# Kernel tuning notes

Measured on AMD Instinct MI355X. Metric: run time of the kernel, lower is better.

## Reference

```python
import jax, jax.numpy as jnp
import numpy as np

N_EMBD = 1024
HEAD_SIZE = 64
BLOCK = 4096
B = 4

def setup_inputs() -> dict:
    key = jax.random.key(0)
    k1, k2, k3, k4, k5, k6 = jax.random.split(key, 6)
    x = jax.random.normal(k1, (B, BLOCK, N_EMBD), dtype=jnp.float32)
    freqs_cos = jax.random.uniform(k2, (BLOCK, HEAD_SIZE // 2), dtype=jnp.float32)
    freqs_sin = jax.random.uniform(k3, (BLOCK, HEAD_SIZE // 2), dtype=jnp.float32)
    # bias-free Linear weights, stored as [in, out] so y = x @ W
    s = 1.0 / np.sqrt(N_EMBD)
    Wq = jax.random.normal(k4, (N_EMBD, HEAD_SIZE), dtype=jnp.float32) * s
    Wk = jax.random.normal(k5, (N_EMBD, HEAD_SIZE), dtype=jnp.float32) * s
    Wv = jax.random.normal(k6, (N_EMBD, HEAD_SIZE), dtype=jnp.float32) * s
    return {"x": x, "Wq": Wq, "Wk": Wk, "Wv": Wv,
            "freqs_cos": freqs_cos, "freqs_sin": freqs_sin}

def _rope(t, cos, sin):
    # t: [B,T,hs]; cos/sin: [T, hs//2]. Rotate consecutive (even,odd) pairs.
    tr = t[..., 0::2]
    ti = t[..., 1::2]
    cos = cos[None, :, :]
    sin = sin[None, :, :]
    out_r = tr * cos - ti * sin
    out_i = tr * sin + ti * cos
    return jnp.stack([out_r, out_i], axis=-1).reshape(t.shape)

def reference(x, Wq, Wk, Wv, freqs_cos, freqs_sin):
    B_, T, C = x.shape
    q = x @ Wq  # [B,T,hs]
    k = x @ Wk
    v = x @ Wv
    q = _rope(q, freqs_cos[:T], freqs_sin[:T])
    k = _rope(k, freqs_cos[:T], freqs_sin[:T])
    scale = k.shape[-1] ** -0.5
    wei = jnp.einsum('bqd,bkd->bqk', q, k) * scale  # [B,T,T]
    mask = jnp.tril(jnp.ones((T, T), dtype=bool))
    wei = jnp.where(mask[None], wei, -jnp.inf)
    wei = jax.nn.softmax(wei, axis=-1)
    return jnp.einsum('bqk,bkd->bqd', wei, v)
```

## Files before the change

### kernel.cpp

```cpp
#include <hip/hip_runtime.h>
#include <stdint.h>

#define TSEQ 4096
#define CEMB 1024
#define DH   64
#define NB   4
#define NCHUNK 4

typedef __attribute__((ext_vector_type(8))) short bf16x8;
typedef __attribute__((ext_vector_type(4))) float f32x4;
typedef __attribute__((ext_vector_type(4))) float f4;
typedef unsigned short u16;

__device__ __forceinline__ u16 f2bf(float f) {
  union { float f; uint32_t u; } c; c.f = f;
  uint32_t u = c.u;
  u += 0x7fffu + ((u >> 16) & 1u);
  return (u16)(u >> 16);
}

__device__ __forceinline__ int swz(int row, int colbyte) {
  return row * 128 + (colbyte ^ ((row & 7) << 4));
}

__global__ void prep_w(const float* __restrict__ Wq, const float* __restrict__ Wk,
                       const float* __restrict__ Wv, u16* __restrict__ wt) {
  int idx = blockIdx.x * 256 + threadIdx.x;
  if (idx >= 3 * DH * CEMB) return;
  int m = idx >> 16;
  int r = idx & 65535;
  int k = r >> 6, n = r & 63;
  const float* W = (m == 0) ? Wq : (m == 1) ? Wk : Wv;
  wt[(size_t)m * 65536 + n * 1024 + k] = f2bf(W[r]);
}

#define QKV_LOADX(K0) { \
    const float* s_ = x + (size_t)(m0 + xrow) * CEMB + (K0) + xc * 8; \
    xa = *(const f4*)s_; xb = *(const f4*)(s_ + 4); }
#define QKV_LOADW(K0) \
    _Pragma("unroll") for (int it = 0; it < 6; ++it) { \
      int gg = it * 256 + tid; \
      wv[it] = *(const bf16x8*)(wt + (size_t)(gg >> 3) * CEMB + (K0) + (gg & 7) * 8); }
#define QKV_STORE(BUF) { \
    bf16x8 xv_; \
    xv_[0] = (short)f2bf(xa[0]); xv_[1] = (short)f2bf(xa[1]); \
    xv_[2] = (short)f2bf(xa[2]); xv_[3] = (short)f2bf(xa[3]); \
    xv_[4] = (short)f2bf(xb[0]); xv_[5] = (short)f2bf(xb[1]); \
    xv_[6] = (short)f2bf(xb[2]); xv_[7] = (short)f2bf(xb[3]); \
    *(bf16x8*)((char*)xs[BUF] + swz(xrow, xc << 4)) = xv_; \
    _Pragma("unroll") for (int it = 0; it < 6; ++it) { \
      int gg = it * 256 + tid; \
      *(bf16x8*)((char*)wsh[BUF] + swz(gg >> 3, (gg & 7) << 4)) = wv[it]; } }

__launch_bounds__(256)
__global__ void qkv_gemm(const float* __restrict__ x, const u16* __restrict__ wt,
                         const float* __restrict__ fc, const float* __restrict__ fs,
                         u16* __restrict__ q_ws, u16* __restrict__ k_ws,
                         u16* __restrict__ vt_ws) {
  __shared__ __align__(16) u16 xs[2][32 * 64];
  __shared__ __align__(16) u16 wsh[2][192 * 64];

  const int tid  = threadIdx.x;
  const int lane = tid & 63;
  const int w    = tid >> 6;
  const int l15  = lane & 15;
  const int lhi  = lane >> 4;
  const int rg   = w & 1;
  const int cg   = w >> 1;
  const int m0   = blockIdx.x * 32;
  const int xrow = tid >> 3, xc = tid & 7;

  const f32x4 z4 = {0.f, 0.f, 0.f, 0.f};
  f32x4 acc[6];
#pragma unroll
  for (int j = 0; j < 6; ++j) acc[j] = z4;

  f4 xa, xb;
  bf16x8 wv[6];

  QKV_LOADX(0)
  QKV_LOADW(0)
  QKV_STORE(0)
  __syncthreads();

  for (int ks = 0; ks < CEMB / 64; ++ks) {
    const int cur  = ks & 1;
    const bool more = (ks + 1 < CEMB / 64);
    if (more) {
      QKV_LOADX((ks + 1) * 64)
      QKV_LOADW((ks + 1) * 64)
    }
#pragma unroll
    for (int kk = 0; kk < 2; ++kk) {
      bf16x8 af = *(const bf16x8*)((char*)xs[cur] + swz(rg * 16 + l15, (kk * 32 + lhi * 8) * 2));
#pragma unroll
      for (int nc = 0; nc < 6; ++nc) {
        bf16x8 bfr = *(const bf16x8*)((char*)wsh[cur] + swz(cg * 96 + nc * 16 + l15, (kk * 32 + lhi * 8) * 2));
        acc[nc] = __builtin_amdgcn_mfma_f32_16x16x32_bf16(af, bfr, acc[nc], 0, 0, 0);
      }
    }
    if (more) QKV_STORE(cur ^ 1)
    __syncthreads();
  }

#pragma unroll
  for (int nc = 0; nc < 6; ++nc) {
    int gcol = cg * 96 + nc * 16 + l15;
    int mat  = gcol >> 6;
    int col  = gcol & 63;
#pragma unroll
    for (int r = 0; r < 4; ++r) {
      float v = acc[nc][r];
      float o = __shfl_xor(v, 1);
      int row = m0 + rg * 16 + lhi * 4 + r;
      int b = row >> 12, t = row & 4095;
      if (mat == 2) {
        vt_ws[((size_t)(b * DH + col)) * TSEQ + t] = f2bf(v);
      } else {
        int p = col >> 1;
        float cv = fc[t * 32 + p], sv = fs[t * 32 + p];
        float outv = ((col & 1) == 0) ? (v * cv - o * sv)
                                      : (o * sv + v * cv);
        u16* dst = (mat == 0) ? q_ws : k_ws;
        dst[(size_t)row * DH + col] = f2bf(outv);
      }
    }
  }
}

#define ATT_LOADKV(KV0) \
    _Pragma("unroll") for (int it = 0; it < 2; ++it) { \
      int gg = it * 256 + tid, row_ = gg >> 3, cc_ = gg & 7; \
      kreg[it] = *(const bf16x8*)(kb + (size_t)((KV0) + row_) * DH + cc_ * 8); \
      vreg[it] = *(const bf16x8*)(vb + (size_t)row_ * TSEQ + (KV0) + cc_ * 8); }
#define ATT_WRITEKV(BUF) \
    _Pragma("unroll") for (int it = 0; it < 2; ++it) { \
      int gg = it * 256 + tid, row_ = gg >> 3, cc_ = gg & 7; \
      *(bf16x8*)((char*)kt[BUF] + swz(row_, cc_ << 4)) = kreg[it]; \
      *(bf16x8*)((char*)vts[BUF] + swz(row_, cc_ << 4)) = vreg[it]; }

__launch_bounds__(256)
__global__ void attn_partial(const u16* __restrict__ q_ws, const u16* __restrict__ k_ws,
                             const u16* __restrict__ vt_ws, float* __restrict__ po,
                             float* __restrict__ pml) {
  const int qt = blockIdx.x;
  const int b  = blockIdx.y;
  const int c  = blockIdx.z;

  const int ntiles = qt + 1;
  const int cnt    = (ntiles + NCHUNK - 1) / NCHUNK;
  const int t0     = c * cnt;
  if (t0 >= ntiles) return;
  const int t1     = min(t0 + cnt, ntiles);
  const int nst    = t1 - t0;

  __shared__ __align__(16) u16 kt[2][64 * 64];
  __shared__ __align__(16) u16 vts[2][64 * 64];
  __shared__ __align__(16) u16 pt2[4 * 16 * 64];

  const int tid  = threadIdx.x;
  const int lane = tid & 63;
  const int w    = tid >> 6;
  const int l15  = lane & 15;
  const int lhi  = lane >> 4;
  const int q0   = qt * 64;

  const u16* qb = q_ws + (size_t)b * TSEQ * DH;
  const u16* kb = k_ws + (size_t)b * TSEQ * DH;
  const u16* vb = vt_ws + (size_t)b * DH * TSEQ;
  char* ptw = (char*)pt2 + w * 2048;

  bf16x8 aq[2];
  {
    int qrow = q0 + w * 16 + l15;
#pragma unroll
    for (int kk = 0; kk < 2; ++kk)
      aq[kk] = *(const bf16x8*)(qb + (size_t)qrow * DH + kk * 32 + lhi * 8);
  }

  const f32x4 z4 = {0.f, 0.f, 0.f, 0.f};
  f32x4 oacc[4] = {z4, z4, z4, z4};
  float m_r[4], l_r[4];
#pragma unroll
  for (int r = 0; r < 4; ++r) { m_r[r] = -1e30f; l_r[r] = 0.f; }

  const int myqbase = q0 + w * 16 + lhi * 4;

  bf16x8 kreg[2], vreg[2];

  ATT_LOADKV(t0 * 64)
  ATT_WRITEKV(0)
  __syncthreads();

  for (int i = 0; i < nst; ++i) {
    const int kv0 = (t0 + i) * 64;
    const int cur = i & 1;
    const bool more = (i + 1 < nst);
    if (more) ATT_LOADKV((t0 + i + 1) * 64)

    f32x4 sacc[4] = {z4, z4, z4, z4};
#pragma unroll
    for (int kk = 0; kk < 2; ++kk) {
#pragma unroll
      for (int cb = 0; cb < 4; ++cb) {
        bf16x8 bk = *(const bf16x8*)((char*)kt[cur] + swz(cb * 16 + l15, (kk * 32 + lhi * 8) * 2));
        sacc[cb] = __builtin_amdgcn_mfma_f32_16x16x32_bf16(aq[kk], bk, sacc[cb], 0, 0, 0);
      }
    }
#pragma unroll
    for (int cb = 0; cb < 4; ++cb)
#pragma unroll
      for (int r = 0; r < 4; ++r) {
        int ki = kv0 + cb * 16 + l15;
        int qi = myqbase + r;
        float sv = sacc[cb][r] * 0.125f;
        sacc[cb][r] = (ki <= qi) ? sv : -1e30f;
      }
    float mx[4];
#pragma unroll
    for (int r = 0; r < 4; ++r)
      mx[r] = fmaxf(fmaxf(sacc[0][r], sacc[1][r]), fmaxf(sacc[2][r], sacc[3][r]));
#pragma unroll
    for (int s = 1; s <= 8; s <<= 1)
#pragma unroll
      for (int r = 0; r < 4; ++r) mx[r] = fmaxf(mx[r], __shfl_xor(mx[r], s));
    float fac[4];
#pragma unroll
    for (int r = 0; r < 4; ++r) {
      float mn = fmaxf(m_r[r], mx[r]);
      fac[r] = __expf(m_r[r] - mn);
      m_r[r] = mn;
    }
    float rs[4] = {0.f, 0.f, 0.f, 0.f};
#pragma unroll
    for (int cb = 0; cb < 4; ++cb)
#pragma unroll
      for (int r = 0; r < 4; ++r) {
        float p = __expf(sacc[cb][r] - m_r[r]);
        sacc[cb][r] = p;
        rs[r] += p;
      }
#pragma unroll
    for (int s = 1; s <= 8; s <<= 1)
#pragma unroll
      for (int r = 0; r < 4; ++r) rs[r] += __shfl_xor(rs[r], s);
#pragma unroll
    for (int r = 0; r < 4; ++r) l_r[r] = l_r[r] * fac[r] + rs[r];
#pragma unroll
    for (int nc = 0; nc < 4; ++nc)
#pragma unroll
      for (int r = 0; r < 4; ++r) oacc[nc][r] *= fac[r];
#pragma unroll
    for (int cb = 0; cb < 4; ++cb)
#pragma unroll
      for (int r = 0; r < 4; ++r)
        *(u16*)(ptw + swz(lhi * 4 + r, (cb * 16 + l15) * 2)) = f2bf(sacc[cb][r]);
    bf16x8 ap[2];
#pragma unroll
    for (int kk = 0; kk < 2; ++kk)
      ap[kk] = *(const bf16x8*)(ptw + swz(l15, (kk * 32 + lhi * 8) * 2));
#pragma unroll
    for (int kk = 0; kk < 2; ++kk)
#pragma unroll
      for (int nc = 0; nc < 4; ++nc) {
        bf16x8 bv = *(const bf16x8*)((char*)vts[cur] + swz(nc * 16 + l15, (kk * 32 + lhi * 8) * 2));
        oacc[nc] = __builtin_amdgcn_mfma_f32_16x16x32_bf16(ap[kk], bv, oacc[nc], 0, 0, 0);
      }

    if (more) ATT_WRITEKV(cur ^ 1)
    __syncthreads();
  }

  const int slot = ((b * 64 + qt) * NCHUNK + c);
  float* o_out = po + (size_t)slot * (64 * 64);
#pragma unroll
  for (int nc = 0; nc < 4; ++nc)
#pragma unroll
    for (int r = 0; r < 4; ++r) {
      int rloc = w * 16 + lhi * 4 + r;
      o_out[rloc * 64 + nc * 16 + l15] = oacc[nc][r];
    }
#pragma unroll
  for (int r = 0; r < 4; ++r) {
    if (l15 == 0) {
      int rloc = w * 16 + lhi * 4 + r;
      pml[(size_t)slot * 128 + rloc]      = m_r[r];
      pml[(size_t)slot * 128 + 64 + rloc] = l_r[r];
    }
  }
}

__launch_bounds__(256)
__global__ void attn_combine(const float* __restrict__ po, const float* __restrict__ pml,
                             float* __restrict__ out) {
  int idx = blockIdx.x * 256 + threadIdx.x;
  int d   = idx & 63;
  int t   = (idx >> 6) & 4095;
  int b   = idx >> 18;
  int qt  = t >> 6;
  int rloc = t & 63;
  int ntiles = qt + 1;
  int cnt = (ntiles + NCHUNK - 1) / NCHUNK;

  float m_c[NCHUNK], l_c[NCHUNK], o_c[NCHUNK];
  float M = -1e30f;
#pragma unroll
  for (int c = 0; c < NCHUNK; ++c) {
    bool valid = (c * cnt < ntiles);
    int slot = ((b * 64 + qt) * NCHUNK + c);
    m_c[c] = valid ? pml[(size_t)slot * 128 + rloc]      : -1e30f;
    l_c[c] = valid ? pml[(size_t)slot * 128 + 64 + rloc] : 0.f;
    o_c[c] = valid ? po[(size_t)slot * (64 * 64) + rloc * 64 + d] : 0.f;
    M = fmaxf(M, m_c[c]);
  }
  float den = 0.f, num = 0.f;
#pragma unroll
  for (int c = 0; c < NCHUNK; ++c) {
    float e = __expf(m_c[c] - M);
    den += e * l_c[c];
    num += e * o_c[c];
  }
  out[idx] = num / den;
}

extern "C" void kernel_launch(void* const* d_in, const int* in_sizes, int n_in,
                              void* d_out, int out_size, void* d_ws, size_t ws_size,
                              hipStream_t stream) {
  const float* x  = (const float*)d_in[0];
  const float* Wq = (const float*)d_in[1];
  const float* Wk = (const float*)d_in[2];
  const float* Wv = (const float*)d_in[3];
  const float* fc = (const float*)d_in[4];
  const float* fs = (const float*)d_in[5];
  float* out = (float*)d_out;

  char* ws = (char*)d_ws;
  u16*   wt    = (u16*)(ws);
  u16*   q_ws  = (u16*)(ws + (1u << 19));
  u16*   k_ws  = (u16*)(ws + (1u << 19) + (1u << 21));
  u16*   vt_ws = (u16*)(ws + (1u << 19) + (2u << 21));
  float* po    = (float*)(ws + (1u << 19) + (3u << 21));
  float* pml   = (float*)(ws + (1u << 19) + (3u << 21) + (1u << 24));

  prep_w<<<(3 * DH * CEMB + 255) / 256, 256, 0, stream>>>(Wq, Wk, Wv, wt);
  qkv_gemm<<<dim3(512), 256, 0, stream>>>(x, wt, fc, fs, q_ws, k_ws, vt_ws);
  attn_partial<<<dim3(64, NB, NCHUNK), 256, 0, stream>>>(q_ws, k_ws, vt_ws, po, pml);
  attn_combine<<<dim3((NB * TSEQ * DH) / 256), 256, 0, stream>>>(po, pml, out);
}
```

Baseline: 180.4 us.

## Rework attention inner loop: lazy rescale, diagonal-only mask, deferred row sums, single buffer

The attention partial kernel moves from double-buffered LDS to a single buffer, with a load, sync, write, sync sequence each iteration. It folds the 1/sqrt(d) scale into Q during the projection and applies the causal mask only on the diagonal tile. Row-sum reductions are deferred to the end of the loop, and the online-softmax rescale is skipped when the new max exceeds the running max by at most 8. It also adds s_setprio around the MFMA blocks and switches bf16 conversion to the HIP intrinsic. Dropping double buffering exposes global load latency, and the lazy rescale lets probabilities grow up to e^8 before they are rounded to bf16.

```diff
diff --git a/kernel.cpp b/kernel.cpp
--- a/kernel.cpp
+++ b/kernel.cpp
@@ -1,4 +1,5 @@
 #include <hip/hip_runtime.h>
+#include <hip/hip_bf16.h>
 #include <stdint.h>
 
 #define TSEQ 4096
@@ -13,10 +14,8 @@
 typedef unsigned short u16;
 
 __device__ __forceinline__ u16 f2bf(float f) {
-  union { float f; uint32_t u; } c; c.f = f;
-  uint32_t u = c.u;
-  u += 0x7fffu + ((u >> 16) & 1u);
-  return (u16)(u >> 16);
+  __hip_bfloat16 h = __float2bfloat16(f);
+  return *(u16*)&h;
 }
 
 __device__ __forceinline__ int swz(int row, int colbyte) {
@@ -121,6 +120,7 @@
         float cv = fc[t * 32 + p], sv = fs[t * 32 + p];
         float outv = ((col & 1) == 0) ? (v * cv - o * sv)
                                       : (o * sv + v * cv);
+        if (mat == 0) outv *= 0.125f;
         u16* dst = (mat == 0) ? q_ws : k_ws;
         dst[(size_t)row * DH + col] = f2bf(outv);
       }
@@ -133,11 +133,11 @@
       int gg = it * 256 + tid, row_ = gg >> 3, cc_ = gg & 7; \
       kreg[it] = *(const bf16x8*)(kb + (size_t)((KV0) + row_) * DH + cc_ * 8); \
       vreg[it] = *(const bf16x8*)(vb + (size_t)row_ * TSEQ + (KV0) + cc_ * 8); }
-#define ATT_WRITEKV(BUF) \
+#define ATT_WRITEKV \
     _Pragma("unroll") for (int it = 0; it < 2; ++it) { \
       int gg = it * 256 + tid, row_ = gg >> 3, cc_ = gg & 7; \
-      *(bf16x8*)((char*)kt[BUF] + swz(row_, cc_ << 4)) = kreg[it]; \
-      *(bf16x8*)((char*)vts[BUF] + swz(row_, cc_ << 4)) = vreg[it]; }
+      *(bf16x8*)((char*)kt + swz(row_, cc_ << 4)) = kreg[it]; \
+      *(bf16x8*)((char*)vts + swz(row_, cc_ << 4)) = vreg[it]; }
 
 __launch_bounds__(256)
 __global__ void attn_partial(const u16* __restrict__ q_ws, const u16* __restrict__ k_ws,
@@ -152,10 +152,9 @@
   const int t0     = c * cnt;
   if (t0 >= ntiles) return;
   const int t1     = min(t0 + cnt, ntiles);
-  const int nst    = t1 - t0;
-
-  __shared__ __align__(16) u16 kt[2][64 * 64];
-  __shared__ __align__(16) u16 vts[2][64 * 64];
+
+  __shared__ __align__(16) u16 kt[64 * 64];
+  __shared__ __align__(16) u16 vts[64 * 64];
   __shared__ __align__(16) u16 pt2[4 * 16 * 64];
 
   const int tid  = threadIdx.x;
@@ -180,42 +179,43 @@
 
   const f32x4 z4 = {0.f, 0.f, 0.f, 0.f};
   f32x4 oacc[4] = {z4, z4, z4, z4};
-  float m_r[4], l_r[4];
-#pragma unroll
-  for (int r = 0; r < 4; ++r) { m_r[r] = -1e30f; l_r[r] = 0.f; }
+  float m_r[4], l_p[4];
+#pragma unroll
+  for (int r = 0; r < 4; ++r) { m_r[r] = -1e30f; l_p[r] = 0.f; }
 
   const int myqbase = q0 + w * 16 + lhi * 4;
 
   bf16x8 kreg[2], vreg[2];
 
-  ATT_LOADKV(t0 * 64)
-  ATT_WRITEKV(0)
-  __syncthreads();
-
-  for (int i = 0; i < nst; ++i) {
-    const int kv0 = (t0 + i) * 64;
-    const int cur = i & 1;
-    const bool more = (i + 1 < nst);
-    if (more) ATT_LOADKV((t0 + i + 1) * 64)
+  for (int kv = t0; kv < t1; ++kv) {
+    const int kv0 = kv * 64;
+    ATT_LOADKV(kv0)
+    __syncthreads();
+    ATT_WRITEKV
+    __syncthreads();
 
     f32x4 sacc[4] = {z4, z4, z4, z4};
+    __builtin_amdgcn_s_setprio(1);
 #pragma unroll
     for (int kk = 0; kk < 2; ++kk) {
 #pragma unroll
       for (int cb = 0; cb < 4; ++cb) {
-        bf16x8 bk = *(const bf16x8*)((char*)kt[cur] + swz(cb * 16 + l15, (kk * 32 + lhi * 8) * 2));
+        bf16x8 bk = *(const bf16x8*)((char*)kt + swz(cb * 16 + l15, (kk * 32 + lhi * 8) * 2));
         sacc[cb] = __builtin_amdgcn_mfma_f32_16x16x32_bf16(aq[kk], bk, sacc[cb], 0, 0, 0);
       }
     }
-#pragma unroll
-    for (int cb = 0; cb < 4; ++cb)
-#pragma unroll
-      for (int r = 0; r < 4; ++r) {
-        int ki = kv0 + cb * 16 + l15;
-        int qi = myqbase + r;
-        float sv = sacc[cb][r] * 0.125f;
-        sacc[cb][r] = (ki <= qi) ? sv : -1e30f;
-      }
+    __builtin_amdgcn_s_setprio(0);
+
+    if (kv0 == q0) {
+#pragma unroll
+      for (int cb = 0; cb < 4; ++cb)
+#pragma unroll
+        for (int r = 0; r < 4; ++r) {
+          int ki = kv0 + cb * 16 + l15;
+          int qi = myqbase + r;
+          if (ki > qi) sacc[cb][r] = -1e30f;
+        }
+    }
     float mx[4];
 #pragma unroll
     for (int r = 0; r < 4; ++r)
@@ -224,52 +224,47 @@
     for (int s = 1; s <= 8; s <<= 1)
 #pragma unroll
       for (int r = 0; r < 4; ++r) mx[r] = fmaxf(mx[r], __shfl_xor(mx[r], s));
-    float fac[4];
-#pragma unroll
-    for (int r = 0; r < 4; ++r) {
-      float mn = fmaxf(m_r[r], mx[r]);
-      fac[r] = __expf(m_r[r] - mn);
-      m_r[r] = mn;
-    }
-    float rs[4] = {0.f, 0.f, 0.f, 0.f};
+    bool skip = true;
+#pragma unroll
+    for (int r = 0; r < 4; ++r) skip = skip && (mx[r] <= m_r[r] + 8.f);
+    if (!__all(skip)) {
+#pragma unroll
+      for (int r = 0; r < 4; ++r) {
+        float mn = fmaxf(m_r[r], mx[r]);
+        float fac = __expf(m_r[r] - mn);
+        m_r[r] = mn;
+        l_p[r] *= fac;
+#pragma unroll
+        for (int nc = 0; nc < 4; ++nc) oacc[nc][r] *= fac;
+      }
+    }
 #pragma unroll
     for (int cb = 0; cb < 4; ++cb)
 #pragma unroll
       for (int r = 0; r < 4; ++r) {
         float p = __expf(sacc[cb][r] - m_r[r]);
-        sacc[cb][r] = p;
-        rs[r] += p;
-      }
-#pragma unroll
-    for (int s = 1; s <= 8; s <<= 1)
-#pragma unroll
-      for (int r = 0; r < 4; ++r) rs[r] += __shfl_xor(rs[r], s);
-#pragma unroll
-    for (int r = 0; r < 4; ++r) l_r[r] = l_r[r] * fac[r] + rs[r];
-#pragma unroll
-    for (int nc = 0; nc < 4; ++nc)
-#pragma unroll
-      for (int r = 0; r < 4; ++r) oacc[nc][r] *= fac[r];
-#pragma unroll
-    for (int cb = 0; cb < 4; ++cb)
-#pragma unroll
-      for (int r = 0; r < 4; ++r)
-        *(u16*)(ptw + swz(lhi * 4 + r, (cb * 16 + l15) * 2)) = f2bf(sacc[cb][r]);
+        l_p[r] += p;
+        *(u16*)(ptw + swz(lhi * 4 + r, (cb * 16 + l15) * 2)) = f2bf(p);
+      }
     bf16x8 ap[2];
 #pragma unroll
     for (int kk = 0; kk < 2; ++kk)
       ap[kk] = *(const bf16x8*)(ptw + swz(l15, (kk * 32 + lhi * 8) * 2));
+    __builtin_amdgcn_s_setprio(1);
 #pragma unroll
     for (int kk = 0; kk < 2; ++kk)
 #pragma unroll
       for (int nc = 0; nc < 4; ++nc) {
-        bf16x8 bv = *(const bf16x8*)((char*)vts[cur] + swz(nc * 16 + l15, (kk * 32 + lhi * 8) * 2));
+        bf16x8 bv = *(const bf16x8*)((char*)vts + swz(nc * 16 + l15, (kk * 32 + lhi * 8) * 2));
         oacc[nc] = __builtin_amdgcn_mfma_f32_16x16x32_bf16(ap[kk], bv, oacc[nc], 0, 0, 0);
       }
-
-    if (more) ATT_WRITEKV(cur ^ 1)
-    __syncthreads();
-  }
+    __builtin_amdgcn_s_setprio(0);
+  }
+
+#pragma unroll
+  for (int s = 1; s <= 8; s <<= 1)
+#pragma unroll
+    for (int r = 0; r < 4; ++r) l_p[r] += __shfl_xor(l_p[r], s);
 
   const int slot = ((b * 64 + qt) * NCHUNK + c);
   float* o_out = po + (size_t)slot * (64 * 64);
@@ -285,7 +280,7 @@
     if (l15 == 0) {
       int rloc = w * 16 + lhi * 4 + r;
       pml[(size_t)slot * 128 + rloc]      = m_r[r];
-      pml[(size_t)slot * 128 + 64 + rloc] = l_r[r];
+      pml[(size_t)slot * 128 + 64 + rloc] = l_p[r];
     }
   }
 }
```

Result: faster. 170.1 us (-5.7%).
